# Kernel optimization log

Hardware: AMD Instinct MI355X
Metric: run time of the kernel (lower is better)

The kernel has to match this reference:

```python
import jax, jax.numpy as jnp
import numpy as np

B, L, M = 64, 2048, 128  # trees, leaves per complete binary tree, mem_dim (== in_dim)


def setup_inputs() -> dict:
    key = jax.random.key(0)
    ks = jax.random.split(key, 16)
    n = lambda k, s, sc=1.0: jax.random.normal(k, s, dtype=jnp.float32) * sc
    W = 0.08  # small init scale for gate weights
    return {
        "embs": n(ks[0], (B, L, M)),
        "root_c": n(ks[1], (B, M)),
        "root_h": n(ks[2], (B, M)),
        "Wi": n(ks[3], (M, M), W), "bi": jnp.zeros((M,), jnp.float32),
        "Wf": n(ks[4], (M, M), W), "bf": jnp.zeros((M,), jnp.float32),
        "Wu": n(ks[5], (M, M), W), "bu": jnp.zeros((M,), jnp.float32),
        "Wc": n(ks[6], (M, M), W), "bc": jnp.zeros((M,), jnp.float32),
        "Wo": n(ks[7], (M, M), W), "bo": jnp.zeros((M,), jnp.float32),
    }


def reference(embs, root_c, root_h, Wi, bi, Wf, bf, Wu, bu, Wc, bc, Wo, bo):
    # Top-down binary-tree LSTM over B complete binary trees, vectorized per level.
    Bn, Ln, Mn = embs.shape
    depth = int(np.log2(Ln))  # root at level 0, leaves at level `depth`

    def composer(pc, ph):
        # BinaryTreeTopDownComposer: gates from parent hidden, cell mixes parent cell
        i = jax.nn.sigmoid(ph @ Wi + bi)
        pf = jax.nn.sigmoid(ph @ Wf + bf)
        u = jnp.tanh(ph @ Wu + bu)
        c = i * u + pf * pc
        return c, jnp.tanh(c)

    def leaf(x):
        # BinaryTreeLeafModule
        c = x @ Wc + bc
        o = jax.nn.sigmoid(x @ Wo + bo)
        return c, o * jnp.tanh(c)

    # root state comes from bp_lstm.root_c / root_h
    pc, ph = root_c[:, None, :], root_h[:, None, :]  # [B, 1, M]
    for _ in range(1, depth):  # internal levels: each node composed from its parent
        pc2 = jnp.repeat(pc, 2, axis=1)  # broadcast parent state to both children
        ph2 = jnp.repeat(ph, 2, axis=1)
        pc, ph = composer(pc2, ph2)

    # leaf level: state = cat(leaf(emb), leaf(parent_h), leaf(parent_c)) along features
    pcl = jnp.repeat(pc, 2, axis=1)  # [B, L, M]
    phl = jnp.repeat(ph, 2, axis=1)
    ce, he = leaf(embs)
    cph, hph = leaf(phl)
    cpc, hpc = leaf(pcl)
    c_leaf = jnp.concatenate([ce, cph, cpc], axis=-1)  # [B, L, 3M]
    h_leaf = jnp.concatenate([he, hph, hpc], axis=-1)  # [B, L, 3M]
    return jnp.concatenate([c_leaf, h_leaf], axis=-1)  # [B, L, 6M]
```

## Files before the change

### kernel.cpp

```cpp
#include <hip/hip_runtime.h>
#include <cstdint>
#include <cstddef>

#define Bb   64
#define Ll   2048
#define Mm   128
#define ROWS (Bb * Ll)
#define OUTC 768
#define LDA  136
#define LDF  132

typedef __attribute__((ext_vector_type(4))) float  f32x4;
typedef __attribute__((ext_vector_type(8))) short  bf16x8;
typedef __attribute__((ext_vector_type(4))) short  short4v;
typedef __bf16 bf16x8b __attribute__((ext_vector_type(8)));

__device__ __forceinline__ float rcp_(float x) {
#if __has_builtin(__builtin_amdgcn_rcpf)
    return __builtin_amdgcn_rcpf(x);
#else
    return 1.0f / x;
#endif
}
__device__ __forceinline__ float sigmoid_(float x) {
    return rcp_(1.0f + __expf(-x));
}
__device__ __forceinline__ float tanh_(float x) {
    float ax = fabsf(x);
    float r  = __expf(-2.0f * ax);
    float t  = (1.0f - r) * rcp_(1.0f + r);
    return x < 0.0f ? -t : t;
}
__device__ __forceinline__ short f2bf(float f) {
    uint32_t u = __builtin_bit_cast(uint32_t, f);
    u = (u + 0x7FFFu + ((u >> 16) & 1u)) >> 16;
    return (short)(u & 0xFFFFu);
}


__global__ __launch_bounds__(512)
void state_kernel(const float* __restrict__ root_c, const float* __restrict__ root_h,
                  const float* __restrict__ Wi, const float* __restrict__ bi,
                  const float* __restrict__ Wf, const float* __restrict__ bfv,
                  const float* __restrict__ Wu, const float* __restrict__ bu,
                  const float* __restrict__ Wc, const float* __restrict__ bc,
                  const float* __restrict__ Wo, const float* __restrict__ bo,
                  float* __restrict__ ws, short* __restrict__ wbf)
{
    const int b   = blockIdx.x;
    const int tid = threadIdx.x;
    const int m   = tid & 127;
    const int q   = tid >> 7;
    const int k0  = q * 32;

    __shared__ float h_sh[Mm];
    __shared__ float c_sh[Mm];
    __shared__ float part[4][4][Mm];

    {
        int idx  = b * 512 + tid;
        int gate = idx >> 14;
        int col  = (idx >> 7) & 127;
        int k    = idx & 127;
        const float* W = gate ? Wo : Wc;
        wbf[idx] = f2bf(W[k * Mm + col]);
    }

    float c = 0.f;
    if (q == 0) {
        c = root_c[b * Mm + m];
        h_sh[m] = root_h[b * Mm + m];
    }
    __syncthreads();

    const float bi_m = bi[m], bf_m = bfv[m], bu_m = bu[m];

    for (int it = 0; it < 10; ++it) {
        float di0 = 0.f, di1 = 0.f, df0 = 0.f, df1 = 0.f, du0 = 0.f, du1 = 0.f;
        #pragma unroll
        for (int kk = 0; kk < 32; kk += 2) {
            int k = k0 + kk;
            float h0 = h_sh[k], h1 = h_sh[k + 1];
            di0 = fmaf(h0, Wi[k * Mm + m], di0);
            di1 = fmaf(h1, Wi[(k + 1) * Mm + m], di1);
            df0 = fmaf(h0, Wf[k * Mm + m], df0);
            df1 = fmaf(h1, Wf[(k + 1) * Mm + m], df1);
            du0 = fmaf(h0, Wu[k * Mm + m], du0);
            du1 = fmaf(h1, Wu[(k + 1) * Mm + m], du1);
        }
        part[0][q][m] = di0 + di1;
        part[1][q][m] = df0 + df1;
        part[2][q][m] = du0 + du1;
        __syncthreads();
        if (q == 0) {
            float di = (part[0][0][m] + part[0][1][m]) + (part[0][2][m] + part[0][3][m]);
            float df = (part[1][0][m] + part[1][1][m]) + (part[1][2][m] + part[1][3][m]);
            float du = (part[2][0][m] + part[2][1][m]) + (part[2][2][m] + part[2][3][m]);
            float ig = sigmoid_(di + bi_m);
            float fg = sigmoid_(df + bf_m);
            float ug = tanh_(du + bu_m);
            c = ig * ug + fg * c;
            h_sh[m] = tanh_(c);
        }
        __syncthreads();
    }
    if (q == 0) c_sh[m] = c;
    __syncthreads();

    float dch = 0.f, doh = 0.f, dcc = 0.f, doc = 0.f;
    #pragma unroll
    for (int kk = 0; kk < 32; ++kk) {
        int k = k0 + kk;
        float hk = h_sh[k], ck = c_sh[k];
        float wc = Wc[k * Mm + m], wo = Wo[k * Mm + m];
        dch = fmaf(hk, wc, dch);
        doh = fmaf(hk, wo, doh);
        dcc = fmaf(ck, wc, dcc);
        doc = fmaf(ck, wo, doc);
    }
    part[0][q][m] = dch;
    part[1][q][m] = doh;
    part[2][q][m] = dcc;
    part[3][q][m] = doc;
    __syncthreads();
    if (q == 0) {
        float Dch = (part[0][0][m] + part[0][1][m]) + (part[0][2][m] + part[0][3][m]);
        float Doh = (part[1][0][m] + part[1][1][m]) + (part[1][2][m] + part[1][3][m]);
        float Dcc = (part[2][0][m] + part[2][1][m]) + (part[2][2][m] + part[2][3][m]);
        float Doc = (part[3][0][m] + part[3][1][m]) + (part[3][2][m] + part[3][3][m]);
        const float bcm = bc[m], bom = bo[m];
        float cph = Dch + bcm;
        float cpc = Dcc + bcm;
        float hph = sigmoid_(Doh + bom) * tanh_(cph);
        float hpc = sigmoid_(Doc + bom) * tanh_(cpc);
        ws[0 * Bb * Mm + b * Mm + m] = cph;
        ws[1 * Bb * Mm + b * Mm + m] = cpc;
        ws[2 * Bb * Mm + b * Mm + m] = hph;
        ws[3 * Bb * Mm + b * Mm + m] = hpc;
    }
}

__global__ __launch_bounds__(512, 4)
void fused_kernel(const float* __restrict__ embs,
                  const short* __restrict__ wbf,
                  const float* __restrict__ bc, const float* __restrict__ bo,
                  const float* __restrict__ state,
                  float* __restrict__ out)
{
    __shared__ __align__(16) char smem[70656];
    short* A0   = (short*)smem;
    short* A1   = (short*)(smem + 17408);
    float* ce_l = (float*)(smem + 34816);
    float* he_l = (float*)(smem + 51712);
    float* st_l = (float*)(smem + 68608);

    const int tid  = threadIdx.x;
    const int w    = tid >> 6;
    const int lane = tid & 63;
    const int g    = lane >> 4;
    const int ln   = lane & 15;
    const int n0   = w * 16 + ln;
    const int rowbase0 = blockIdx.x * 128;
    const int rowbase1 = rowbase0 + 64;
    const int b        = rowbase0 >> 11;

    bf16x8 bfrag[2][4];
    #pragma unroll
    for (int gate = 0; gate < 2; ++gate)
        #pragma unroll
        for (int ks = 0; ks < 4; ++ks)
            bfrag[gate][ks] = *(const bf16x8*)(
                wbf + gate * (Mm * Mm) + n0 * Mm + ks * 32 + g * 8);
    const float biasc = bc[n0];
    const float biaso = bo[n0];
    st_l[tid] = state[(tid >> 7) * (Bb * Mm) + b * Mm + (tid & 127)];

    auto stage_load = [&](int rowbase, f32x4 (&r)[4]) {
        #pragma unroll
        for (int i = 0; i < 4; ++i) {
            int idx = tid + 512 * i;
            int rr  = idx >> 5;
            int kq  = idx & 31;
            r[i] = __builtin_nontemporal_load(
                (const f32x4*)(embs + (size_t)(rowbase + rr) * Mm + kq * 4));
        }
    };
    auto stage_write = [&](short* A, const f32x4 (&r)[4]) {
        #pragma unroll
        for (int i = 0; i < 4; ++i) {
            int idx = tid + 512 * i;
            int rr  = idx >> 5;
            int kq  = idx & 31;
            short4v s4;
            s4[0] = f2bf(r[i][0]); s4[1] = f2bf(r[i][1]);
            s4[2] = f2bf(r[i][2]); s4[3] = f2bf(r[i][3]);
            *(short4v*)(&A[rr * LDA + kq * 4]) = s4;
        }
    };
    auto do_mfma = [&](const short* A, f32x4 (&acc)[4][2]) {
        #pragma unroll
        for (int rt = 0; rt < 4; ++rt)
            #pragma unroll
            for (int gate = 0; gate < 2; ++gate) {
                float bv = gate ? biaso : biasc;
                acc[rt][gate][0] = bv; acc[rt][gate][1] = bv;
                acc[rt][gate][2] = bv; acc[rt][gate][3] = bv;
            }
        #pragma unroll
        for (int ks = 0; ks < 4; ++ks) {
            bf16x8 af[4];
            #pragma unroll
            for (int rt = 0; rt < 4; ++rt)
                af[rt] = *(const bf16x8*)(&A[(rt * 16 + ln) * LDA + ks * 32 + g * 8]);
            #pragma unroll
            for (int rt = 0; rt < 4; ++rt)
                #pragma unroll
                for (int gate = 0; gate < 2; ++gate)
                    acc[rt][gate] = __builtin_amdgcn_mfma_f32_16x16x32_bf16(
                        __builtin_bit_cast(bf16x8b, af[rt]),
                        __builtin_bit_cast(bf16x8b, bfrag[gate][ks]),
                        acc[rt][gate], 0, 0, 0);
        }
    };
    auto epilogue = [&](int rowbase, f32x4 (&acc)[4][2]) {
        #pragma unroll
        for (int half = 0; half < 2; ++half) {
            #pragma unroll
            for (int qq = 0; qq < 2; ++qq) {
                int rt = half * 2 + qq;
                #pragma unroll
                for (int r = 0; r < 4; ++r) {
                    int rowL = qq * 16 + g * 4 + r;
                    float cv = acc[rt][0][r];
                    float hv = sigmoid_(acc[rt][1][r]) * tanh_(cv);
                    ce_l[rowL * LDF + n0] = cv;
                    he_l[rowL * LDF + n0] = hv;
                }
            }
            __syncthreads();
            #pragma unroll
            for (int i = 0; i < 12; ++i) {
                int u  = tid + 512 * i;
                int rg = u / 192;
                int s  = u - rg * 192;
                int sec = s >> 5;
                int cc  = s & 31;
                const float* src =
                    (sec == 0) ? (ce_l + rg * LDF + cc * 4) :
                    (sec == 3) ? (he_l + rg * LDF + cc * 4) :
                    (st_l + ((sec < 3) ? (sec - 1) : (sec - 2)) * 128 + cc * 4);
                f32x4 v = *(const f32x4*)src;
                *(f32x4*)(out + (size_t)(rowbase + half * 32 + rg) * OUTC + s * 4) = v;
            }
            __syncthreads();
        }
    };

    f32x4 r0[4], r1[4];
    f32x4 acc[4][2];

    stage_load(rowbase0, r0);
    stage_write(A0, r0);
    __syncthreads();

    stage_load(rowbase1, r1);

    do_mfma(A0, acc);
    stage_write(A1, r1);
    __syncthreads();

    epilogue(rowbase0, acc);
    do_mfma(A1, acc);
    epilogue(rowbase1, acc);
}

extern "C" void kernel_launch(void* const* d_in, const int* in_sizes, int n_in,
                              void* d_out, int out_size, void* d_ws, size_t ws_size,
                              hipStream_t stream) {
    const float* embs   = (const float*)d_in[0];
    const float* root_c = (const float*)d_in[1];
    const float* root_h = (const float*)d_in[2];
    const float* Wi = (const float*)d_in[3];
    const float* bi = (const float*)d_in[4];
    const float* Wf = (const float*)d_in[5];
    const float* bfv= (const float*)d_in[6];
    const float* Wu = (const float*)d_in[7];
    const float* bu = (const float*)d_in[8];
    const float* Wc = (const float*)d_in[9];
    const float* bc = (const float*)d_in[10];
    const float* Wo = (const float*)d_in[11];
    const float* bo = (const float*)d_in[12];

    float* out   = (float*)d_out;
    float* state = (float*)d_ws;
    short* wbf   = (short*)d_ws + 65536;

    state_kernel<<<dim3(Bb), dim3(512), 0, stream>>>(
        root_c, root_h, Wi, bi, Wf, bfv, Wu, bu, Wc, bc, Wo, bo, state, wbf);
    fused_kernel<<<dim3(1024), dim3(512), 0, stream>>>(
        embs, wbf, bc, bo, state, out);
}
```

Measured before the change: 110.4 us.

## Swap MFMA operands so each wave owns rows and writes output directly from registers

Restructures the fused leaf kernel so each wave loads its own 16 embedding rows straight into registers as the MFMA B operand, while the weights move to a swizzled shared-memory buffer as the A operand. Results land in row-major fragments and are stored to global directly, removing the LDS staging of activations and outputs and most of the block barriers. Each block now handles 256 rows with a register prefetch of the second tile, halving the grid. The trade-offs are more LDS reads for weights per MFMA, narrower per-lane stores, and a larger shared footprint for the full weight matrix.

```diff
diff --git a/kernel.cpp b/kernel.cpp
--- a/kernel.cpp
+++ b/kernel.cpp
@@ -7,12 +7,9 @@
 #define Mm   128
 #define ROWS (Bb * Ll)
 #define OUTC 768
-#define LDA  136
-#define LDF  132
 
 typedef __attribute__((ext_vector_type(4))) float  f32x4;
 typedef __attribute__((ext_vector_type(8))) short  bf16x8;
-typedef __attribute__((ext_vector_type(4))) short  short4v;
 typedef __bf16 bf16x8b __attribute__((ext_vector_type(8)));
 
 __device__ __forceinline__ float rcp_(float x) {
@@ -147,131 +144,107 @@
                   const float* __restrict__ state,
                   float* __restrict__ out)
 {
-    __shared__ __align__(16) char smem[70656];
-    short* A0   = (short*)smem;
-    short* A1   = (short*)(smem + 17408);
-    float* ce_l = (float*)(smem + 34816);
-    float* he_l = (float*)(smem + 51712);
-    float* st_l = (float*)(smem + 68608);
+    __shared__ __align__(16) char smem[66560];
+    char*  Wsw    = smem;
+    float* bias_l = (float*)(smem + 65536);
 
     const int tid  = threadIdx.x;
     const int w    = tid >> 6;
     const int lane = tid & 63;
     const int g    = lane >> 4;
     const int ln   = lane & 15;
-    const int n0   = w * 16 + ln;
-    const int rowbase0 = blockIdx.x * 128;
-    const int rowbase1 = rowbase0 + 64;
-    const int b        = rowbase0 >> 11;
-
-    bf16x8 bfrag[2][4];
-    #pragma unroll
-    for (int gate = 0; gate < 2; ++gate)
-        #pragma unroll
-        for (int ks = 0; ks < 4; ++ks)
-            bfrag[gate][ks] = *(const bf16x8*)(
-                wbf + gate * (Mm * Mm) + n0 * Mm + ks * 32 + g * 8);
-    const float biasc = bc[n0];
-    const float biaso = bo[n0];
-    st_l[tid] = state[(tid >> 7) * (Bb * Mm) + b * Mm + (tid & 127)];
-
-    auto stage_load = [&](int rowbase, f32x4 (&r)[4]) {
-        #pragma unroll
-        for (int i = 0; i < 4; ++i) {
-            int idx = tid + 512 * i;
-            int rr  = idx >> 5;
-            int kq  = idx & 31;
-            r[i] = __builtin_nontemporal_load(
-                (const f32x4*)(embs + (size_t)(rowbase + rr) * Mm + kq * 4));
-        }
-    };
-    auto stage_write = [&](short* A, const f32x4 (&r)[4]) {
-        #pragma unroll
-        for (int i = 0; i < 4; ++i) {
-            int idx = tid + 512 * i;
-            int rr  = idx >> 5;
-            int kq  = idx & 31;
-            short4v s4;
-            s4[0] = f2bf(r[i][0]); s4[1] = f2bf(r[i][1]);
-            s4[2] = f2bf(r[i][2]); s4[3] = f2bf(r[i][3]);
-            *(short4v*)(&A[rr * LDA + kq * 4]) = s4;
-        }
-    };
-    auto do_mfma = [&](const short* A, f32x4 (&acc)[4][2]) {
-        #pragma unroll
-        for (int rt = 0; rt < 4; ++rt)
-            #pragma unroll
-            for (int gate = 0; gate < 2; ++gate) {
-                float bv = gate ? biaso : biasc;
-                acc[rt][gate][0] = bv; acc[rt][gate][1] = bv;
-                acc[rt][gate][2] = bv; acc[rt][gate][3] = bv;
+    const int block_row = blockIdx.x * 256;
+    const int b         = block_row >> 11;
+
+    f32x4 e0[4], e1[4];
+    {
+        const float* erow = embs + (size_t)(block_row + w * 16 + ln) * Mm;
+        #pragma unroll
+        for (int ks = 0; ks < 4; ++ks) {
+            e0[ks] = __builtin_nontemporal_load((const f32x4*)(erow + ks * 32 + g * 8));
+            e1[ks] = __builtin_nontemporal_load((const f32x4*)(erow + ks * 32 + g * 8 + 4));
+        }
+    }
+
+    #pragma unroll
+    for (int i = 0; i < 8; ++i) {
+        int s = tid + 512 * i;
+        bf16x8 v = *(const bf16x8*)(wbf + s * 8);
+        int byteoff = ((s >> 4) << 8) | (((s & 15) ^ ((s >> 4) & 15)) << 4);
+        *(bf16x8*)(Wsw + byteoff) = v;
+    }
+    if (tid < 256) bias_l[tid] = (tid < 128) ? bc[tid] : bo[tid - 128];
+
+    f32x4 sv[4];
+    #pragma unroll
+    for (int s = 0; s < 4; ++s)
+        sv[s] = *(const f32x4*)(state + s * (Bb * Mm) + b * Mm + (lane >> 1) * 4);
+
+    __syncthreads();
+
+    #pragma unroll
+    for (int it = 0; it < 2; ++it) {
+        const int rowb = block_row + it * 128 + w * 16;
+
+        bf16x8 ef[4];
+        #pragma unroll
+        for (int ks = 0; ks < 4; ++ks) {
+            bf16x8 f;
+            f[0] = f2bf(e0[ks][0]); f[1] = f2bf(e0[ks][1]);
+            f[2] = f2bf(e0[ks][2]); f[3] = f2bf(e0[ks][3]);
+            f[4] = f2bf(e1[ks][0]); f[5] = f2bf(e1[ks][1]);
+            f[6] = f2bf(e1[ks][2]); f[7] = f2bf(e1[ks][3]);
+            ef[ks] = f;
+        }
+        if (it == 0) {
+            const float* erow = embs + (size_t)(rowb + 128 + ln) * Mm;
+            #pragma unroll
+            for (int ks = 0; ks < 4; ++ks) {
+                e0[ks] = __builtin_nontemporal_load((const f32x4*)(erow + ks * 32 + g * 8));
+                e1[ks] = __builtin_nontemporal_load((const f32x4*)(erow + ks * 32 + g * 8 + 4));
             }
-        #pragma unroll
-        for (int ks = 0; ks < 4; ++ks) {
-            bf16x8 af[4];
-            #pragma unroll
-            for (int rt = 0; rt < 4; ++rt)
-                af[rt] = *(const bf16x8*)(&A[(rt * 16 + ln) * LDA + ks * 32 + g * 8]);
-            #pragma unroll
-            for (int rt = 0; rt < 4; ++rt)
-                #pragma unroll
-                for (int gate = 0; gate < 2; ++gate)
-                    acc[rt][gate] = __builtin_amdgcn_mfma_f32_16x16x32_bf16(
-                        __builtin_bit_cast(bf16x8b, af[rt]),
-                        __builtin_bit_cast(bf16x8b, bfrag[gate][ks]),
-                        acc[rt][gate], 0, 0, 0);
-        }
-    };
-    auto epilogue = [&](int rowbase, f32x4 (&acc)[4][2]) {
-        #pragma unroll
-        for (int half = 0; half < 2; ++half) {
-            #pragma unroll
-            for (int qq = 0; qq < 2; ++qq) {
-                int rt = half * 2 + qq;
-                #pragma unroll
-                for (int r = 0; r < 4; ++r) {
-                    int rowL = qq * 16 + g * 4 + r;
-                    float cv = acc[rt][0][r];
-                    float hv = sigmoid_(acc[rt][1][r]) * tanh_(cv);
-                    ce_l[rowL * LDF + n0] = cv;
-                    he_l[rowL * LDF + n0] = hv;
-                }
+        }
+
+        float* orow = out + (size_t)(rowb + ln) * OUTC;
+
+        #pragma unroll
+        for (int cc = 0; cc < 8; ++cc) {
+            f32x4 accc = *(const f32x4*)(bias_l + cc * 16 + g * 4);
+            f32x4 acco = *(const f32x4*)(bias_l + 128 + cc * 16 + g * 4);
+            #pragma unroll
+            for (int ks = 0; ks < 4; ++ks) {
+                const bf16x8* wp = (const bf16x8*)(Wsw +
+                    (((cc * 16 + ln) << 8) | ((((ks * 4 + g) ^ ln)) << 4)));
+                accc = __builtin_amdgcn_mfma_f32_16x16x32_bf16(
+                    __builtin_bit_cast(bf16x8b, *wp),
+                    __builtin_bit_cast(bf16x8b, ef[ks]), accc, 0, 0, 0);
             }
-            __syncthreads();
-            #pragma unroll
-            for (int i = 0; i < 12; ++i) {
-                int u  = tid + 512 * i;
-                int rg = u / 192;
-                int s  = u - rg * 192;
-                int sec = s >> 5;
-                int cc  = s & 31;
-                const float* src =
-                    (sec == 0) ? (ce_l + rg * LDF + cc * 4) :
-                    (sec == 3) ? (he_l + rg * LDF + cc * 4) :
-                    (st_l + ((sec < 3) ? (sec - 1) : (sec - 2)) * 128 + cc * 4);
-                f32x4 v = *(const f32x4*)src;
-                *(f32x4*)(out + (size_t)(rowbase + half * 32 + rg) * OUTC + s * 4) = v;
+            #pragma unroll
+            for (int ks = 0; ks < 4; ++ks) {
+                const bf16x8* wp = (const bf16x8*)(Wsw +
+                    (((128 + cc * 16 + ln) << 8) | ((((ks * 4 + g) ^ ln)) << 4)));
+                acco = __builtin_amdgcn_mfma_f32_16x16x32_bf16(
+                    __builtin_bit_cast(bf16x8b, *wp),
+                    __builtin_bit_cast(bf16x8b, ef[ks]), acco, 0, 0, 0);
             }
-            __syncthreads();
-        }
-    };
-
-    f32x4 r0[4], r1[4];
-    f32x4 acc[4][2];
-
-    stage_load(rowbase0, r0);
-    stage_write(A0, r0);
-    __syncthreads();
-
-    stage_load(rowbase1, r1);
-
-    do_mfma(A0, acc);
-    stage_write(A1, r1);
-    __syncthreads();
-
-    epilogue(rowbase0, acc);
-    do_mfma(A1, acc);
-    epilogue(rowbase1, acc);
+            f32x4 hv;
+            #pragma unroll
+            for (int r = 0; r < 4; ++r)
+                hv[r] = sigmoid_(acco[r]) * tanh_(accc[r]);
+            *(f32x4*)(orow + cc * 16 + g * 4)       = accc;
+            *(f32x4*)(orow + 384 + cc * 16 + g * 4) = hv;
+        }
+
+        #pragma unroll
+        for (int i = 0; i < 8; ++i) {
+            float* br = out + (size_t)(rowb + 2 * i + (lane & 1)) * OUTC
+                            + (lane >> 1) * 4;
+            *(f32x4*)(br + 128) = sv[0];
+            *(f32x4*)(br + 256) = sv[1];
+            *(f32x4*)(br + 512) = sv[2];
+            *(f32x4*)(br + 640) = sv[3];
+        }
+    }
 }
 
 extern "C" void kernel_launch(void* const* d_in, const int* in_sizes, int n_in,
@@ -297,6 +270,6 @@
 
     state_kernel<<<dim3(Bb), dim3(512), 0, stream>>>(
         root_c, root_h, Wi, bi, Wf, bfv, Wu, bu, Wc, bc, Wo, bo, state, wbf);
-    fused_kernel<<<dim3(1024), dim3(512), 0, stream>>>(
+    fused_kernel<<<dim3(512), dim3(512), 0, stream>>>(
         embs, wbf, bc, bo, state, out);
 }
```

Measured after the change: 125.7 us. 13.8% more time.

## Loop fused kernel over four row tiles with double buffering and direct state stores

Applied to the files above, without the earlier changes.

The fused kernel now handles 256 rows per block in a four-step loop, alternating two LDS buffers so the next tile's global load and bf16 conversion overlap the current tile's MFMAs, and it launches half as many blocks. The parent-state columns are written straight from registers instead of being staged through the shared transpose, which shrinks the LDS-staged epilogue. __syncthreads is replaced by an inline-asm lgkmcnt wait plus barrier. The state kernel also caches its gate weight columns in registers across the ten levels. Fewer blocks on a 256-CU part may lower occupancy, and the custom barrier does not wait on outstanding global memory operations.

```diff
diff --git a/kernel.cpp b/kernel.cpp
--- a/kernel.cpp
+++ b/kernel.cpp
@@ -35,6 +35,10 @@
     uint32_t u = __builtin_bit_cast(uint32_t, f);
     u = (u + 0x7FFFu + ((u >> 16) & 1u)) >> 16;
     return (short)(u & 0xFFFFu);
+}
+
+__device__ __forceinline__ void lds_sync() {
+    asm volatile("s_waitcnt lgkmcnt(0)\n\ts_barrier" ::: "memory");
 }
 
 
@@ -66,6 +70,14 @@
         wbf[idx] = f2bf(W[k * Mm + col]);
     }
 
+    float wi[32], wf[32], wu[32];
+    #pragma unroll
+    for (int kk = 0; kk < 32; ++kk) {
+        wi[kk] = Wi[(k0 + kk) * Mm + m];
+        wf[kk] = Wf[(k0 + kk) * Mm + m];
+        wu[kk] = Wu[(k0 + kk) * Mm + m];
+    }
+
     float c = 0.f;
     if (q == 0) {
         c = root_c[b * Mm + m];
@@ -79,14 +91,13 @@
         float di0 = 0.f, di1 = 0.f, df0 = 0.f, df1 = 0.f, du0 = 0.f, du1 = 0.f;
         #pragma unroll
         for (int kk = 0; kk < 32; kk += 2) {
-            int k = k0 + kk;
-            float h0 = h_sh[k], h1 = h_sh[k + 1];
-            di0 = fmaf(h0, Wi[k * Mm + m], di0);
-            di1 = fmaf(h1, Wi[(k + 1) * Mm + m], di1);
-            df0 = fmaf(h0, Wf[k * Mm + m], df0);
-            df1 = fmaf(h1, Wf[(k + 1) * Mm + m], df1);
-            du0 = fmaf(h0, Wu[k * Mm + m], du0);
-            du1 = fmaf(h1, Wu[(k + 1) * Mm + m], du1);
+            float h0 = h_sh[k0 + kk], h1 = h_sh[k0 + kk + 1];
+            di0 = fmaf(h0, wi[kk], di0);
+            di1 = fmaf(h1, wi[kk + 1], di1);
+            df0 = fmaf(h0, wf[kk], df0);
+            df1 = fmaf(h1, wf[kk + 1], df1);
+            du0 = fmaf(h0, wu[kk], du0);
+            du1 = fmaf(h1, wu[kk + 1], du1);
         }
         part[0][q][m] = di0 + di1;
         part[1][q][m] = df0 + df1;
@@ -160,9 +171,8 @@
     const int g    = lane >> 4;
     const int ln   = lane & 15;
     const int n0   = w * 16 + ln;
-    const int rowbase0 = blockIdx.x * 128;
-    const int rowbase1 = rowbase0 + 64;
-    const int b        = rowbase0 >> 11;
+    const int block_row = blockIdx.x * 256;
+    const int b         = block_row >> 11;
 
     bf16x8 bfrag[2][4];
     #pragma unroll
@@ -175,14 +185,14 @@
     const float biaso = bo[n0];
     st_l[tid] = state[(tid >> 7) * (Bb * Mm) + b * Mm + (tid & 127)];
 
-    auto stage_load = [&](int rowbase, f32x4 (&r)[4]) {
+    auto stage_load = [&](int rb, f32x4 (&r)[4]) {
         #pragma unroll
         for (int i = 0; i < 4; ++i) {
             int idx = tid + 512 * i;
             int rr  = idx >> 5;
             int kq  = idx & 31;
             r[i] = __builtin_nontemporal_load(
-                (const f32x4*)(embs + (size_t)(rowbase + rr) * Mm + kq * 4));
+                (const f32x4*)(embs + (size_t)(rb + rr) * Mm + kq * 4));
         }
     };
     auto stage_write = [&](short* A, const f32x4 (&r)[4]) {
@@ -197,7 +207,20 @@
             *(short4v*)(&A[rr * LDA + kq * 4]) = s4;
         }
     };
-    auto do_mfma = [&](const short* A, f32x4 (&acc)[4][2]) {
+
+    f32x4 r[4];
+    stage_load(block_row, r);
+    stage_write(A0, r);
+    lds_sync();
+
+    for (int t = 0; t < 4; ++t) {
+        const int rowbase = block_row + t * 64;
+        const short* Acur = (t & 1) ? A1 : A0;
+        short*       Anxt = (t & 1) ? A0 : A1;
+
+        if (t < 3) stage_load(rowbase + 64, r);
+
+        f32x4 acc[4][2];
         #pragma unroll
         for (int rt = 0; rt < 4; ++rt)
             #pragma unroll
@@ -211,7 +234,7 @@
             bf16x8 af[4];
             #pragma unroll
             for (int rt = 0; rt < 4; ++rt)
-                af[rt] = *(const bf16x8*)(&A[(rt * 16 + ln) * LDA + ks * 32 + g * 8]);
+                af[rt] = *(const bf16x8*)(&Acur[(rt * 16 + ln) * LDA + ks * 32 + g * 8]);
             #pragma unroll
             for (int rt = 0; rt < 4; ++rt)
                 #pragma unroll
@@ -221,57 +244,58 @@
                         __builtin_bit_cast(bf16x8b, bfrag[gate][ks]),
                         acc[rt][gate], 0, 0, 0);
         }
-    };
-    auto epilogue = [&](int rowbase, f32x4 (&acc)[4][2]) {
+
+        if (t < 3) stage_write(Anxt, r);
+
         #pragma unroll
         for (int half = 0; half < 2; ++half) {
             #pragma unroll
             for (int qq = 0; qq < 2; ++qq) {
                 int rt = half * 2 + qq;
                 #pragma unroll
-                for (int r = 0; r < 4; ++r) {
-                    int rowL = qq * 16 + g * 4 + r;
-                    float cv = acc[rt][0][r];
-                    float hv = sigmoid_(acc[rt][1][r]) * tanh_(cv);
+                for (int rr = 0; rr < 4; ++rr) {
+                    int rowL = qq * 16 + g * 4 + rr;
+                    float cv = acc[rt][0][rr];
+                    float hv = sigmoid_(acc[rt][1][rr]) * tanh_(cv);
                     ce_l[rowL * LDF + n0] = cv;
                     he_l[rowL * LDF + n0] = hv;
                 }
             }
-            __syncthreads();
-            #pragma unroll
-            for (int i = 0; i < 12; ++i) {
-                int u  = tid + 512 * i;
-                int rg = u / 192;
-                int s  = u - rg * 192;
+            lds_sync();
+            #pragma unroll
+            for (int i = 0; i < 4; ++i) {
+                int u   = tid + 512 * i;
+                int rg  = u >> 6;
+                int s   = u & 63;
                 int sec = s >> 5;
                 int cc  = s & 31;
-                const float* src =
-                    (sec == 0) ? (ce_l + rg * LDF + cc * 4) :
-                    (sec == 3) ? (he_l + rg * LDF + cc * 4) :
-                    (st_l + ((sec < 3) ? (sec - 1) : (sec - 2)) * 128 + cc * 4);
+                const float* src = (sec ? he_l : ce_l) + rg * LDF + cc * 4;
                 f32x4 v = *(const f32x4*)src;
-                *(f32x4*)(out + (size_t)(rowbase + half * 32 + rg) * OUTC + s * 4) = v;
+                *(f32x4*)(out + (size_t)(rowbase + half * 32 + rg) * OUTC
+                              + sec * 384 + cc * 4) = v;
             }
-            __syncthreads();
-        }
-    };
-
-    f32x4 r0[4], r1[4];
-    f32x4 acc[4][2];
-
-    stage_load(rowbase0, r0);
-    stage_write(A0, r0);
-    __syncthreads();
-
-    stage_load(rowbase1, r1);
-
-    do_mfma(A0, acc);
-    stage_write(A1, r1);
-    __syncthreads();
-
-    epilogue(rowbase0, acc);
-    do_mfma(A1, acc);
-    epilogue(rowbase1, acc);
+            if (half == 0) lds_sync();
+        }
+
+        {
+            int c4 = (tid & 31) * 4;
+            int rw = tid >> 5;
+            f32x4 s0 = *(const f32x4*)(st_l + 0 * 128 + c4);
+            f32x4 s1 = *(const f32x4*)(st_l + 1 * 128 + c4);
+            f32x4 s2 = *(const f32x4*)(st_l + 2 * 128 + c4);
+            f32x4 s3 = *(const f32x4*)(st_l + 3 * 128 + c4);
+            #pragma unroll
+            for (int j = 0; j < 4; ++j) {
+                float* br = out + (size_t)(rowbase + rw + 16 * j) * OUTC + c4;
+                *(f32x4*)(br + 128) = s0;
+                *(f32x4*)(br + 256) = s1;
+                *(f32x4*)(br + 512) = s2;
+                *(f32x4*)(br + 640) = s3;
+            }
+        }
+
+        lds_sync();
+    }
 }
 
 extern "C" void kernel_launch(void* const* d_in, const int* in_sizes, int n_in,
@@ -297,6 +321,6 @@
 
     state_kernel<<<dim3(Bb), dim3(512), 0, stream>>>(
         root_c, root_h, Wi, bi, Wf, bfv, Wu, bu, Wc, bc, Wo, bo, state, wbf);
-    fused_kernel<<<dim3(1024), dim3(512), 0, stream>>>(
+    fused_kernel<<<dim3(512), dim3(512), 0, stream>>>(
         embs, wbf, bc, bo, state, out);
 }
```

Result: slower. 115.6 us (+4.7%).
